# Kernel tuning notes

Hardware: AMD Instinct MI355X
Metric: run time of the kernel (lower is better)

The kernel has to match this reference:

```python
import jax, jax.numpy as jnp
import numpy as np

B, L, H, E, MODES = 32, 2048, 8, 64, 64
SCALE = 1.0 / (512 * 512)  # 1/(in_channels*out_channels)


def setup_inputs() -> dict:
    key = jax.random.key(0)
    kq, kk, kv, kwr, kwi = jax.random.split(key, 5)
    # frequency mode selection: shuffled range(L//2), first MODES, sorted (get_frequency_modes)
    rng = np.random.default_rng(0)
    index = np.sort(rng.permutation(L // 2)[:MODES]).astype(np.int32)
    return {
        "q": jax.random.normal(kq, (B, L, H, E), dtype=jnp.float32),
        "k": jax.random.normal(kk, (B, L, H, E), dtype=jnp.float32),
        "v": jax.random.normal(kv, (B, L, H, E), dtype=jnp.float32),
        "w_real": SCALE * jax.random.uniform(kwr, (H, E, E, MODES), dtype=jnp.float32),
        "w_imag": SCALE * jax.random.uniform(kwi, (H, E, E, MODES), dtype=jnp.float32),
        "index": jnp.asarray(index),
    }


def reference(q, k, v, w_real, w_imag, index):
    # q: [B, L, H, E]; k, v unused by FourierBlock
    Bq, Lq, Hq, Eq = q.shape
    x = jnp.transpose(q, (0, 2, 3, 1))            # [B, H, E, L]
    x_ft = jnp.fft.rfft(x, axis=-1)               # [B, H, E, L//2+1] complex
    xs = jnp.take(x_ft, index, axis=-1)           # gather selected modes: [B, H, E, M]
    W = w_real + 1j * w_imag                      # [H, E, E, M] complex
    # vectorized per-mode complex einsum ('bhi,hio->bho' over all modes m)
    out = jnp.einsum('bhim,hiom->bhom', xs, W)    # [B, H, E, M]
    n_freq = Lq // 2 + 1
    # original writes mode wi into slot wi (0..M-1), rest stay zero
    out_ft = jnp.concatenate(
        [out, jnp.zeros((Bq, Hq, Eq, n_freq - out.shape[-1]), dtype=out.dtype)], axis=-1)
    return jnp.fft.irfft(out_ft, n=Lq, axis=-1)   # [B, H, E, L] real
```

## Files before the change

### kernel.cpp

```cpp
#include <hip/hip_runtime.h>
#include <math.h>

#define NB 32
#define NL 2048
#define NH 8
#define NE 64
#define NM 64
#define MRI 128
#define BK 128
#define NCH 16

typedef __attribute__((ext_vector_type(8))) __bf16 bf16x8;
typedef __attribute__((ext_vector_type(2))) __bf16 bf16x2;
typedef __attribute__((ext_vector_type(8))) unsigned short us8;
typedef __attribute__((ext_vector_type(4))) unsigned short us4;
typedef __attribute__((ext_vector_type(4))) float f32x4;
typedef __attribute__((ext_vector_type(16))) float f32x16;

__device__ __forceinline__ unsigned short f2bf(float x) {
  unsigned int u = __builtin_bit_cast(unsigned int, x);
  u = (u + 0x7fffu + ((u >> 16) & 1u)) >> 16;
  return (unsigned short)u;
}
__device__ __forceinline__ float bf2f(unsigned short u) {
  return __builtin_bit_cast(float, (unsigned int)u << 16);
}
__device__ __forceinline__ unsigned int pk2(float lo, float hi) {
  bf16x2 v;
  v[0] = (__bf16)lo;
  v[1] = (__bf16)hi;
  return __builtin_bit_cast(unsigned int, v);
}

__global__ void tables_k(const int* __restrict__ idx,
                         const float* __restrict__ wr, const float* __restrict__ wi,
                         unsigned short* __restrict__ Tf, unsigned short* __restrict__ IT,
                         unsigned short* __restrict__ WBr, unsigned short* __restrict__ WBi) {
  int gid = blockIdx.x * blockDim.x + threadIdx.x;
  const float w0 = 6.283185307179586f / (float)NL;
  {
    int j = gid & 7, lane_ = (gid >> 3) & 63, tm_ = (gid >> 9) & 3;
    int ks_ = (gid >> 11) & 3, kh_ = (gid >> 13) & 1, c_ = gid >> 14;
    int row = tm_ * 32 + (lane_ & 31);
    int m = row & 63;
    int k = c_ * 128 + kh_ * 64 + ks_ * 16 + (lane_ >> 5) * 8 + j;
    int f = idx[m];
    float s, c2;
    sincosf((float)((f * k) & (NL - 1)) * w0, &s, &c2);
    Tf[gid] = f2bf(row < 64 ? c2 : -s);
  }
  {
    int lp = gid >> 7, k = gid & 127;
    int m = k & 63;
    float s, c;
    sincosf((float)((m * lp) & (NL - 1)) * w0, &s, &c);
    float v = (k < 64) ? ((m == 0 ? 1.0f : 2.0f) / (float)NL) * c
                       : (m == 0 ? 0.0f : (-2.0f / (float)NL) * s);
    IT[gid] = f2bf(v);
  }
  {
    const float2* wr2 = (const float2*)wr;
    const float2* wi2 = (const float2*)wi;
    unsigned int* obr = (unsigned int*)WBr;
    unsigned int* obi = (unsigned int*)WBi;
#pragma unroll
    for (int r = 0; r < 4; ++r) {
      int j = r * 262144 + gid;
      float2 a = wr2[j];
      float2 b2 = wi2[j];
      obr[j] = pk2(a.x, a.y);
      obi[j] = pk2(b2.x, b2.y);
    }
  }
}

__global__ __launch_bounds__(1024) void fused_k(const float* __restrict__ q,
                                                const unsigned short* __restrict__ T,
                                                const unsigned short* __restrict__ IT,
                                                const unsigned short* __restrict__ WBr,
                                                const unsigned short* __restrict__ WBi,
                                                float* __restrict__ out) {
  __shared__ __align__(16) char smem[84992];
  int t = threadIdx.x, lane = t & 63, wid = t >> 6;
  int h = blockIdx.x & 7, b = blockIdx.x >> 3;

  {
    char* B0 = smem + 51200;
    char* B1 = smem + 51200 + 16896;
    const float* qb = q + ((size_t)b * NL * NH + h) * NE;
    int tm = wid & 3;
    int te = (wid >> 2) & 1;
    int kh = wid >> 3;
    int eq = t & 15, lq = t >> 4;
    f32x16 acc32 = {};
    f32x4 qA[2], qB[2];
    us8 arA[4], arB[4];

    auto qload = [&](int c, f32x4* qr) {
#pragma unroll
      for (int p = 0; p < 2; ++p)
        qr[p] = *(const f32x4*)(qb + (size_t)(c * BK + lq * 2 + p) * (NH * NE) + eq * 4);
    };
    auto writesB = [&](const f32x4* qr, char* bb) {
#pragma unroll
      for (int j = 0; j < 4; ++j) {
        int e = eq * 4 + j;
        *(unsigned int*)(bb + e * 264 + lq * 4) = pk2(qr[0][j], qr[1][j]);
      }
    };
    auto loadAreg = [&](int c, us8* ar) {
#pragma unroll
      for (int ks = 0; ks < 4; ++ks)
        ar[ks] = *(const us8*)(T + ((((size_t)c * 2 + kh) * 4 + ks) * 4 + tm) * 512 + lane * 8);
    };
    auto compute = [&](const us8* ar, const char* bb) {
#pragma unroll
      for (int ks = 0; ks < 4; ++ks) {
        int k0 = (kh * 4 + ks) * 16;
        int e = te * 32 + (lane & 31);
        int boff = e * 264 + (k0 + (lane >> 5) * 8) * 2;
        uint2 blo = *(const uint2*)(bb + boff);
        uint2 bhi = *(const uint2*)(bb + boff + 8);
        bf16x8 bfr = __builtin_bit_cast(bf16x8, make_uint4(blo.x, blo.y, bhi.x, bhi.y));
        acc32 = __builtin_amdgcn_mfma_f32_32x32x16_bf16(
            __builtin_bit_cast(bf16x8, ar[ks]), bfr, acc32, 0, 0, 0);
      }
    };

    qload(0, qA);
    qload(1, qB);
    loadAreg(0, arA);
    writesB(qA, B0);
    asm volatile("s_waitcnt lgkmcnt(0)" ::: "memory");
    __builtin_amdgcn_s_barrier();
    for (int c = 0; c < 16; c += 2) {
      loadAreg(c + 1, arB);
      if (c + 2 < 16) qload(c + 2, qA);
      compute(arA, B0);
      __builtin_amdgcn_s_barrier();
      writesB(qB, B1);
      asm volatile("s_waitcnt lgkmcnt(0)" ::: "memory");
      __builtin_amdgcn_s_barrier();
      if (c + 2 < 16) loadAreg(c + 2, arA);
      if (c + 3 < 16) qload(c + 3, qB);
      compute(arB, B1);
      if (c + 2 < 16) {
        __builtin_amdgcn_s_barrier();
        writesB(qA, B0);
        asm volatile("s_waitcnt lgkmcnt(0)" ::: "memory");
        __builtin_amdgcn_s_barrier();
      }
    }
    __syncthreads();

    float* scr = (float*)(smem + 51200);
    int tile = wid & 7;
    if (kh == 1) {
#pragma unroll
      for (int r = 0; r < 16; ++r) {
        int row = (r & 3) + 8 * (r >> 2) + 4 * (lane >> 5);
        scr[tile * 1024 + row * 32 + (lane & 31)] = acc32[r];
      }
    }
    __syncthreads();
    if (kh == 0) {
#pragma unroll
      for (int r = 0; r < 16; ++r) {
        int row = (r & 3) + 8 * (r >> 2) + 4 * (lane >> 5);
        float v = acc32[r] + scr[tile * 1024 + row * 32 + (lane & 31)];
        int grow = tm * 32 + row;
        int gcol = te * 32 + (lane & 31);
        int off = (grow * 272 + gcol * 4) ^ (((grow >> 3) & 7) << 4);
        *(float*)(smem + off) = v;
      }
    }
  }
  __syncthreads();

  {
    char* OtB = smem + 34816;
    int o = t >> 4, mq = t & 15;
    const unsigned short* wbr = WBr + (size_t)h * 262144 + o * 64 + mq * 4;
    const unsigned short* wbi = WBi + (size_t)h * 262144 + o * 64 + mq * 4;
    float orr[4] = {}, oii[4] = {};
#pragma unroll 2
    for (int ib = 0; ib < 16; ++ib) {
      f32x4 xr4[4], xi4[4];
#pragma unroll
      for (int mi = 0; mi < 4; ++mi) {
        int m = mq * 4 + mi;
        xr4[mi] = *(const f32x4*)(smem + ((m * 272 + ib * 16) ^ (((m >> 3) & 7) << 4)));
        xi4[mi] = *(const f32x4*)(smem + (((64 + m) * 272 + ib * 16) ^ (((m >> 3) & 7) << 4)));
      }
      us4 wr4[4], wi4[4];
#pragma unroll
      for (int ii = 0; ii < 4; ++ii) {
        int i = ib * 4 + ii;
        wr4[ii] = *(const us4*)(wbr + (size_t)i * 4096);
        wi4[ii] = *(const us4*)(wbi + (size_t)i * 4096);
      }
#pragma unroll
      for (int ii = 0; ii < 4; ++ii)
#pragma unroll
        for (int mi = 0; mi < 4; ++mi) {
          float wrv = bf2f(wr4[ii][mi]);
          float wiv = bf2f(wi4[ii][mi]);
          orr[mi] += xr4[mi][ii] * wrv - xi4[mi][ii] * wiv;
          oii[mi] += xr4[mi][ii] * wiv + xi4[mi][ii] * wrv;
        }
    }
    uint2 vr = make_uint2(pk2(orr[0], orr[1]), pk2(orr[2], orr[3]));
    uint2 vi = make_uint2(pk2(oii[0], oii[1]), pk2(oii[2], oii[3]));
    *(uint2*)(OtB + ((o * 256 + mq * 8) ^ ((o & 7) << 4))) = vr;
    *(uint2*)(OtB + ((o * 256 + 128 + mq * 8) ^ ((o & 7) << 4))) = vi;
  }
  __syncthreads();

  {
    const char* OtB = smem + 34816;
    bf16x8 af[2][8];
#pragma unroll
    for (int rg2 = 0; rg2 < 2; ++rg2)
#pragma unroll
      for (int ks = 0; ks < 8; ++ks) {
        int row = rg2 * 32 + (lane & 31);
        int off = (row * 256 + ks * 32 + (lane >> 5) * 16) ^ ((row & 7) << 4);
        af[rg2][ks] = __builtin_bit_cast(bf16x8, *(const us8*)(OtB + off));
      }
    float* ob = out + ((size_t)(b * 8 + h) * 64) * NL;
    int l0 = wid * 128;
    for (int ct = 0; ct < 4; ++ct) {
      int lr = l0 + ct * 32 + (lane & 31);
      f32x16 a2[2] = {};
#pragma unroll
      for (int ks = 0; ks < 8; ++ks) {
        bf16x8 bv = __builtin_bit_cast(
            bf16x8, *(const us8*)(IT + (size_t)lr * MRI + ks * 16 + (lane >> 5) * 8));
        a2[0] = __builtin_amdgcn_mfma_f32_32x32x16_bf16(af[0][ks], bv, a2[0], 0, 0, 0);
        a2[1] = __builtin_amdgcn_mfma_f32_32x32x16_bf16(af[1][ks], bv, a2[1], 0, 0, 0);
      }
#pragma unroll
      for (int rg2 = 0; rg2 < 2; ++rg2)
#pragma unroll
        for (int rg = 0; rg < 16; ++rg) {
          int row = rg2 * 32 + ((rg & 3) + 8 * (rg >> 2) + 4 * (lane >> 5));
          ob[(size_t)row * NL + lr] = a2[rg2][rg];
        }
    }
  }
}

extern "C" void kernel_launch(void* const* d_in, const int* in_sizes, int n_in,
                              void* d_out, int out_size, void* d_ws, size_t ws_size,
                              hipStream_t stream) {
  const float* q = (const float*)d_in[0];
  const float* wr = (const float*)d_in[3];
  const float* wi = (const float*)d_in[4];
  const int* idx = (const int*)d_in[5];
  float* out = (float*)d_out;
  char* ws = (char*)d_ws;

  constexpr size_t TBYTES = (size_t)MRI * NL * 2;
  constexpr size_t WBBYTES = (size_t)NH * NE * NE * NM * 2;
  constexpr size_t NEED = 2 * TBYTES + 2 * WBBYTES;
  if (ws_size < NEED) return;

  unsigned short* Tf = (unsigned short*)ws;
  unsigned short* IT = (unsigned short*)(ws + TBYTES);
  unsigned short* WBr = (unsigned short*)(ws + 2 * TBYTES);
  unsigned short* WBi = (unsigned short*)(ws + 2 * TBYTES + WBBYTES);

  hipLaunchKernelGGL(tables_k, dim3(1024), dim3(256), 0, stream, idx, wr, wi, Tf, IT, WBr, WBi);
  hipLaunchKernelGGL(fused_k, dim3(NB * NH), dim3(1024), 0, stream, q, Tf, IT, WBr, WBi, out);
}
```

Measured before the change: 93.87 us.

## Load q directly into MFMA B-operand registers, dropping LDS staging and barriers

The forward DFT GEMM no longer stages q tiles through shared memory with packed bf16 writes and block barriers. Each lane now gathers its eight scalar q values straight from global memory per k-step, converts them to bf16 and feeds the MFMA directly, with double-buffered registers. This removes LDS traffic and barrier stalls, at the cost of uncoalesced scalar global loads (stride NH*NE floats across rows) and duplicated loads across the waves that share the same e-range.

```diff
diff --git a/kernel.cpp b/kernel.cpp
--- a/kernel.cpp
+++ b/kernel.cpp
@@ -80,75 +80,60 @@
                                                 const unsigned short* __restrict__ WBr,
                                                 const unsigned short* __restrict__ WBi,
                                                 float* __restrict__ out) {
-  __shared__ __align__(16) char smem[84992];
+  __shared__ __align__(16) char smem[83968];
   int t = threadIdx.x, lane = t & 63, wid = t >> 6;
   int h = blockIdx.x & 7, b = blockIdx.x >> 3;
 
   {
-    char* B0 = smem + 51200;
-    char* B1 = smem + 51200 + 16896;
     const float* qb = q + ((size_t)b * NL * NH + h) * NE;
     int tm = wid & 3;
     int te = (wid >> 2) & 1;
     int kh = wid >> 3;
-    int eq = t & 15, lq = t >> 4;
+    int e0 = te * 32 + (lane & 31);
+    int loff = (lane >> 5) * 8;
     f32x16 acc32 = {};
-    f32x4 qA[2], qB[2];
     us8 arA[4], arB[4];
-
-    auto qload = [&](int c, f32x4* qr) {
-#pragma unroll
-      for (int p = 0; p < 2; ++p)
-        qr[p] = *(const f32x4*)(qb + (size_t)(c * BK + lq * 2 + p) * (NH * NE) + eq * 4);
-    };
-    auto writesB = [&](const f32x4* qr, char* bb) {
-#pragma unroll
-      for (int j = 0; j < 4; ++j) {
-        int e = eq * 4 + j;
-        *(unsigned int*)(bb + e * 264 + lq * 4) = pk2(qr[0][j], qr[1][j]);
-      }
-    };
-    auto loadAreg = [&](int c, us8* ar) {
+    bf16x8 bfA[4], bfB[4];
+
+    auto loadA = [&](int c, us8* ar) {
 #pragma unroll
       for (int ks = 0; ks < 4; ++ks)
         ar[ks] = *(const us8*)(T + ((((size_t)c * 2 + kh) * 4 + ks) * 4 + tm) * 512 + lane * 8);
     };
-    auto compute = [&](const us8* ar, const char* bb) {
+    auto loadB = [&](int c, bf16x8* bf) {
 #pragma unroll
       for (int ks = 0; ks < 4; ++ks) {
-        int k0 = (kh * 4 + ks) * 16;
-        int e = te * 32 + (lane & 31);
-        int boff = e * 264 + (k0 + (lane >> 5) * 8) * 2;
-        uint2 blo = *(const uint2*)(bb + boff);
-        uint2 bhi = *(const uint2*)(bb + boff + 8);
-        bf16x8 bfr = __builtin_bit_cast(bf16x8, make_uint4(blo.x, blo.y, bhi.x, bhi.y));
+        float tmp[8];
+#pragma unroll
+        for (int j = 0; j < 8; ++j)
+          tmp[j] = qb[(size_t)(c * BK + kh * 64 + ks * 16 + loff + j) * (NH * NE) + e0];
+        bf16x8 v;
+#pragma unroll
+        for (int j = 0; j < 8; ++j) v[j] = (__bf16)tmp[j];
+        bf[ks] = v;
+      }
+    };
+    auto compute = [&](const us8* ar, const bf16x8* bf) {
+#pragma unroll
+      for (int ks = 0; ks < 4; ++ks)
         acc32 = __builtin_amdgcn_mfma_f32_32x32x16_bf16(
-            __builtin_bit_cast(bf16x8, ar[ks]), bfr, acc32, 0, 0, 0);
-      }
+            __builtin_bit_cast(bf16x8, ar[ks]), bf[ks], acc32, 0, 0, 0);
     };
 
-    qload(0, qA);
-    qload(1, qB);
-    loadAreg(0, arA);
-    writesB(qA, B0);
-    asm volatile("s_waitcnt lgkmcnt(0)" ::: "memory");
-    __builtin_amdgcn_s_barrier();
+    loadA(0, arA);
+    loadB(0, bfA);
+    loadA(1, arB);
+    loadB(1, bfB);
     for (int c = 0; c < 16; c += 2) {
-      loadAreg(c + 1, arB);
-      if (c + 2 < 16) qload(c + 2, qA);
-      compute(arA, B0);
-      __builtin_amdgcn_s_barrier();
-      writesB(qB, B1);
-      asm volatile("s_waitcnt lgkmcnt(0)" ::: "memory");
-      __builtin_amdgcn_s_barrier();
-      if (c + 2 < 16) loadAreg(c + 2, arA);
-      if (c + 3 < 16) qload(c + 3, qB);
-      compute(arB, B1);
+      compute(arA, bfA);
       if (c + 2 < 16) {
-        __builtin_amdgcn_s_barrier();
-        writesB(qA, B0);
-        asm volatile("s_waitcnt lgkmcnt(0)" ::: "memory");
-        __builtin_amdgcn_s_barrier();
+        loadA(c + 2, arA);
+        loadB(c + 2, bfA);
+      }
+      compute(arB, bfB);
+      if (c + 3 < 16) {
+        loadA(c + 3, arB);
+        loadB(c + 3, bfB);
       }
     }
     __syncthreads();
```

After: 104.5 us. 1.11x slower.

## Double the DFT K-chunk to 256, swizzle LDS B tile, use nontemporal output stores

Applied to the files above, without the earlier changes.

Raises the forward-DFT chunk size from 128 to 256 time samples, which halves the number of pipeline iterations and barriers. The twiddle-table layout and the per-thread register buffers (q and A fragments) double to match. The shared-memory B tile changes from padded rows to an XOR-swizzled layout, so each MFMA operand comes from a single 16-byte LDS read. Final output writes become nontemporal stores. The trade-off is more LDS (about 114KB) and more VGPRs per thread, which may pressure a 1024-thread block.

```diff
diff --git a/kernel.cpp b/kernel.cpp
--- a/kernel.cpp
+++ b/kernel.cpp
@@ -7,8 +7,8 @@
 #define NE 64
 #define NM 64
 #define MRI 128
-#define BK 128
-#define NCH 16
+#define BK 256
+#define NCH 8
 
 typedef __attribute__((ext_vector_type(8))) __bf16 bf16x8;
 typedef __attribute__((ext_vector_type(2))) __bf16 bf16x2;
@@ -40,10 +40,10 @@
   const float w0 = 6.283185307179586f / (float)NL;
   {
     int j = gid & 7, lane_ = (gid >> 3) & 63, tm_ = (gid >> 9) & 3;
-    int ks_ = (gid >> 11) & 3, kh_ = (gid >> 13) & 1, c_ = gid >> 14;
+    int ks_ = (gid >> 11) & 7, kh_ = (gid >> 14) & 1, c_ = gid >> 15;
     int row = tm_ * 32 + (lane_ & 31);
     int m = row & 63;
-    int k = c_ * 128 + kh_ * 64 + ks_ * 16 + (lane_ >> 5) * 8 + j;
+    int k = c_ * 256 + kh_ * 128 + ks_ * 16 + (lane_ >> 5) * 8 + j;
     int f = idx[m];
     float s, c2;
     sincosf((float)((f * k) & (NL - 1)) * w0, &s, &c2);
@@ -80,48 +80,48 @@
                                                 const unsigned short* __restrict__ WBr,
                                                 const unsigned short* __restrict__ WBi,
                                                 float* __restrict__ out) {
-  __shared__ __align__(16) char smem[84992];
+  __shared__ __align__(16) char smem[116736];
   int t = threadIdx.x, lane = t & 63, wid = t >> 6;
   int h = blockIdx.x & 7, b = blockIdx.x >> 3;
 
   {
     char* B0 = smem + 51200;
-    char* B1 = smem + 51200 + 16896;
+    char* B1 = smem + 51200 + 32768;
     const float* qb = q + ((size_t)b * NL * NH + h) * NE;
     int tm = wid & 3;
     int te = (wid >> 2) & 1;
     int kh = wid >> 3;
     int eq = t & 15, lq = t >> 4;
     f32x16 acc32 = {};
-    f32x4 qA[2], qB[2];
-    us8 arA[4], arB[4];
+    f32x4 qA[4], qB[4];
+    us8 arA[8], arB[8];
 
     auto qload = [&](int c, f32x4* qr) {
 #pragma unroll
-      for (int p = 0; p < 2; ++p)
-        qr[p] = *(const f32x4*)(qb + (size_t)(c * BK + lq * 2 + p) * (NH * NE) + eq * 4);
+      for (int p = 0; p < 4; ++p)
+        qr[p] = *(const f32x4*)(qb + (size_t)(c * BK + lq * 4 + p) * (NH * NE) + eq * 4);
     };
     auto writesB = [&](const f32x4* qr, char* bb) {
 #pragma unroll
       for (int j = 0; j < 4; ++j) {
         int e = eq * 4 + j;
-        *(unsigned int*)(bb + e * 264 + lq * 4) = pk2(qr[0][j], qr[1][j]);
-      }
-    };
-    auto loadAreg = [&](int c, us8* ar) {
-#pragma unroll
-      for (int ks = 0; ks < 4; ++ks)
-        ar[ks] = *(const us8*)(T + ((((size_t)c * 2 + kh) * 4 + ks) * 4 + tm) * 512 + lane * 8);
+        int sw = (e & 31) << 4;
+        *(uint2*)(bb + ((e * 512 + lq * 8) ^ sw)) =
+            make_uint2(pk2(qr[0][j], qr[1][j]), pk2(qr[2][j], qr[3][j]));
+      }
+    };
+    auto loadA = [&](int c, us8* ar) {
+#pragma unroll
+      for (int ks = 0; ks < 8; ++ks)
+        ar[ks] = *(const us8*)(T + ((((size_t)c * 2 + kh) * 8 + ks) * 4 + tm) * 512 + lane * 8);
     };
     auto compute = [&](const us8* ar, const char* bb) {
 #pragma unroll
-      for (int ks = 0; ks < 4; ++ks) {
-        int k0 = (kh * 4 + ks) * 16;
+      for (int ks = 0; ks < 8; ++ks) {
         int e = te * 32 + (lane & 31);
-        int boff = e * 264 + (k0 + (lane >> 5) * 8) * 2;
-        uint2 blo = *(const uint2*)(bb + boff);
-        uint2 bhi = *(const uint2*)(bb + boff + 8);
-        bf16x8 bfr = __builtin_bit_cast(bf16x8, make_uint4(blo.x, blo.y, bhi.x, bhi.y));
+        int kbyte = (kh * 128 + ks * 16 + (lane >> 5) * 8) * 2;
+        int boff = (e * 512 + kbyte) ^ ((e & 31) << 4);
+        bf16x8 bfr = __builtin_bit_cast(bf16x8, *(const us8*)(bb + boff));
         acc32 = __builtin_amdgcn_mfma_f32_32x32x16_bf16(
             __builtin_bit_cast(bf16x8, ar[ks]), bfr, acc32, 0, 0, 0);
       }
@@ -129,22 +129,22 @@
 
     qload(0, qA);
     qload(1, qB);
-    loadAreg(0, arA);
+    loadA(0, arA);
     writesB(qA, B0);
     asm volatile("s_waitcnt lgkmcnt(0)" ::: "memory");
     __builtin_amdgcn_s_barrier();
-    for (int c = 0; c < 16; c += 2) {
-      loadAreg(c + 1, arB);
-      if (c + 2 < 16) qload(c + 2, qA);
+    for (int c = 0; c < NCH; c += 2) {
+      loadA(c + 1, arB);
+      if (c + 2 < NCH) qload(c + 2, qA);
       compute(arA, B0);
       __builtin_amdgcn_s_barrier();
       writesB(qB, B1);
       asm volatile("s_waitcnt lgkmcnt(0)" ::: "memory");
       __builtin_amdgcn_s_barrier();
-      if (c + 2 < 16) loadAreg(c + 2, arA);
-      if (c + 3 < 16) qload(c + 3, qB);
+      if (c + 2 < NCH) loadA(c + 2, arA);
+      if (c + 3 < NCH) qload(c + 3, qB);
       compute(arB, B1);
-      if (c + 2 < 16) {
+      if (c + 2 < NCH) {
         __builtin_amdgcn_s_barrier();
         writesB(qA, B0);
         asm volatile("s_waitcnt lgkmcnt(0)" ::: "memory");
@@ -244,7 +244,7 @@
 #pragma unroll
         for (int rg = 0; rg < 16; ++rg) {
           int row = rg2 * 32 + ((rg & 3) + 8 * (rg >> 2) + 4 * (lane >> 5));
-          ob[(size_t)row * NL + lr] = a2[rg2][rg];
+          __builtin_nontemporal_store(a2[rg2][rg], &ob[(size_t)row * NL + lr]);
         }
     }
   }
```

Result: faster. 84.33 us (-10.2%).

## Triple-buffer Q staging in LDS to drop a barrier per chunk; nontemporal output stores

Applied to the files above, without the earlier changes.

Switches the forward-DFT GEMM's LDS B-buffers from double to triple buffering with a rotating pointer set. This lets the write of the next chunk overlap the current compute without the extra barrier before each write, and adds sched_barriers to keep the loads ahead of the MFMAs. LDS usage grows slightly and the other stage buffers are relocated to fit. Final output stores become nontemporal to avoid polluting cache.

```diff
diff --git a/kernel.cpp b/kernel.cpp
--- a/kernel.cpp
+++ b/kernel.cpp
@@ -80,13 +80,14 @@
                                                 const unsigned short* __restrict__ WBr,
                                                 const unsigned short* __restrict__ WBi,
                                                 float* __restrict__ out) {
-  __shared__ __align__(16) char smem[84992];
+  __shared__ __align__(16) char smem[85504];
   int t = threadIdx.x, lane = t & 63, wid = t >> 6;
   int h = blockIdx.x & 7, b = blockIdx.x >> 3;
 
   {
-    char* B0 = smem + 51200;
-    char* B1 = smem + 51200 + 16896;
+    char* bC = smem + 34816;
+    char* bN = smem + 34816 + 16896;
+    char* bX = smem + 34816 + 33792;
     const float* qb = q + ((size_t)b * NL * NH + h) * NE;
     int tm = wid & 3;
     int te = (wid >> 2) & 1;
@@ -108,7 +109,7 @@
         *(unsigned int*)(bb + e * 264 + lq * 4) = pk2(qr[0][j], qr[1][j]);
       }
     };
-    auto loadAreg = [&](int c, us8* ar) {
+    auto loadA = [&](int c, us8* ar) {
 #pragma unroll
       for (int ks = 0; ks < 4; ++ks)
         ar[ks] = *(const us8*)(T + ((((size_t)c * 2 + kh) * 4 + ks) * 4 + tm) * 512 + lane * 8);
@@ -126,34 +127,42 @@
             __builtin_bit_cast(bf16x8, ar[ks]), bfr, acc32, 0, 0, 0);
       }
     };
+    auto rot = [&]() {
+      char* tmp = bC;
+      bC = bN;
+      bN = bX;
+      bX = tmp;
+    };
 
     qload(0, qA);
     qload(1, qB);
-    loadAreg(0, arA);
-    writesB(qA, B0);
+    loadA(0, arA);
+    writesB(qA, bC);
     asm volatile("s_waitcnt lgkmcnt(0)" ::: "memory");
     __builtin_amdgcn_s_barrier();
-    for (int c = 0; c < 16; c += 2) {
-      loadAreg(c + 1, arB);
-      if (c + 2 < 16) qload(c + 2, qA);
-      compute(arA, B0);
-      __builtin_amdgcn_s_barrier();
-      writesB(qB, B1);
+    for (int c = 0; c < NCH; c += 2) {
+      loadA(c + 1, arB);
+      if (c + 2 < NCH) qload(c + 2, qA);
+      __builtin_amdgcn_sched_barrier(0);
+      compute(arA, bC);
+      writesB(qB, bN);
       asm volatile("s_waitcnt lgkmcnt(0)" ::: "memory");
       __builtin_amdgcn_s_barrier();
-      if (c + 2 < 16) loadAreg(c + 2, arA);
-      if (c + 3 < 16) qload(c + 3, qB);
-      compute(arB, B1);
-      if (c + 2 < 16) {
-        __builtin_amdgcn_s_barrier();
-        writesB(qA, B0);
+      rot();
+      if (c + 2 < NCH) loadA(c + 2, arA);
+      if (c + 3 < NCH) qload(c + 3, qB);
+      __builtin_amdgcn_sched_barrier(0);
+      compute(arB, bC);
+      if (c + 2 < NCH) {
+        writesB(qA, bN);
         asm volatile("s_waitcnt lgkmcnt(0)" ::: "memory");
         __builtin_amdgcn_s_barrier();
       }
+      rot();
     }
     __syncthreads();
 
-    float* scr = (float*)(smem + 51200);
+    float* scr = (float*)(smem + 34816);
     int tile = wid & 7;
     if (kh == 1) {
 #pragma unroll
@@ -178,7 +187,7 @@
   __syncthreads();
 
   {
-    char* OtB = smem + 34816;
+    char* OtB = smem + 67584;
     int o = t >> 4, mq = t & 15;
     const unsigned short* wbr = WBr + (size_t)h * 262144 + o * 64 + mq * 4;
     const unsigned short* wbi = WBi + (size_t)h * 262144 + o * 64 + mq * 4;
@@ -217,7 +226,7 @@
   __syncthreads();
 
   {
-    const char* OtB = smem + 34816;
+    const char* OtB = smem + 67584;
     bf16x8 af[2][8];
 #pragma unroll
     for (int rg2 = 0; rg2 < 2; ++rg2)
@@ -244,7 +253,7 @@
 #pragma unroll
         for (int rg = 0; rg < 16; ++rg) {
           int row = rg2 * 32 + ((rg & 3) + 8 * (rg >> 2) + 4 * (lane >> 5));
-          ob[(size_t)row * NL + lr] = a2[rg2][rg];
+          __builtin_nontemporal_store(a2[rg2][rg], &ob[(size_t)row * NL + lr]);
         }
     }
   }
```

Result: faster. 82.61 us (-12.0%).
